# Kernel optimization log

Measured on AMD Instinct MI355X. Metric: run time of the kernel, lower is better.

The kernel has to match this reference:

```python
import jax, jax.numpy as jnp
import numpy as np

H, HKV, D, T, S, HID, I = 16, 8, 128, 2048, 4096, 2048, 8192
EPS = 1e-6
SCALE = 1.0 / (D ** 0.5)
NREP = H // HKV


def _rope_tables():
    inv_freq = 1.0 / (10000.0 ** (np.arange(0, D, 2, dtype=np.float32) / D))
    pos = np.arange(T, dtype=np.float32)
    freqs = np.outer(pos, inv_freq)            # (T, D/2)
    emb = np.concatenate([freqs, freqs], -1)   # (T, D)
    return jnp.asarray(np.cos(emb))[None], jnp.asarray(np.sin(emb))[None]


def setup_inputs() -> dict:
    key = jax.random.key(0)
    ks = jax.random.split(key, 8)
    w = 0.02
    cos, sin = _rope_tables()
    # causal mask over the full cache: query i may attend key j iff j <= i (current_pos=0)
    i = jnp.arange(T)[:, None]
    j = jnp.arange(S)[None, :]
    causal_mask = jnp.where(j <= i, 0.0, -1e9).astype(jnp.float32)[None, None]
    return {
        "hidden_conv": jax.random.normal(ks[0], (1, HID, 1, T), jnp.float32),
        "cos": cos, "sin": sin,
        "causal_mask": causal_mask,
        "kv_cache": jnp.zeros((2, HKV, S, D), jnp.float32),
        "wq": jax.random.normal(ks[1], (H * D, HID), jnp.float32) * w,
        "wk": jax.random.normal(ks[2], (HKV * D, HID), jnp.float32) * w,
        "wv": jax.random.normal(ks[3], (HKV * D, HID), jnp.float32) * w,
        "wo": jax.random.normal(ks[4], (H * D, HID), jnp.float32).T * w,  # (HID, H*D) stored as (out,in)
        "w_gate_up": jax.random.normal(ks[5], (2 * I, HID), jnp.float32) * w,
        "w_down": jax.random.normal(ks[6], (HID, I), jnp.float32) * w,
        "input_ln_w": jnp.ones((HID,), jnp.float32),
        "post_ln_w": jnp.ones((HID,), jnp.float32),
        "q_norm_w": jnp.ones((D,), jnp.float32),
        "k_norm_w": jnp.ones((D,), jnp.float32),
        "current_pos": 0,
    }


def _rms(x, w):
    return x * jax.lax.rsqrt(jnp.mean(x * x, axis=-1, keepdims=True) + EPS) * w


def _rot_half(x):
    x1, x2 = jnp.split(x, 2, axis=-1)
    return jnp.concatenate([-x2, x1], axis=-1)


def _layer(hidden_conv, cos, sin, causal_mask, kv_cache, wq, wk, wv, wo,
           w_gate_up, w_down, input_ln_w, post_ln_w, q_norm_w, k_norm_w, current_pos):
    x = hidden_conv[0, :, 0, :].T                       # (T, HID)
    h = _rms(x, input_ln_w)
    q = (h @ wq.T).reshape(T, H, D).transpose(1, 0, 2)   # (H, T, D)
    k = (h @ wk.T).reshape(T, HKV, D).transpose(1, 0, 2) # (HKV, T, D)
    v = (h @ wv.T).reshape(T, HKV, D).transpose(1, 0, 2)
    q = _rms(q, q_norm_w)
    k = _rms(k, k_norm_w)
    c, s = cos[0], sin[0]                                # (T, D)
    q = q * c + _rot_half(q) * s
    k = k * c + _rot_half(k) * s
    kv = kv_cache.at[0, :, current_pos:current_pos + T, :].set(k)
    kv = kv.at[1, :, current_pos:current_pos + T, :].set(v)
    k_rep = jnp.repeat(kv[0], NREP, axis=0)              # (H, S, D)
    v_rep = jnp.repeat(kv[1], NREP, axis=0)
    scores = jnp.einsum('htd,hsd->hts', q, k_rep) * SCALE + causal_mask[0, 0]
    attn = jax.nn.softmax(scores, axis=-1)
    out = jnp.einsum('hts,hsd->htd', attn, v_rep)        # (H, T, D)
    out = out.transpose(1, 0, 2).reshape(T, H * D)
    hidden = x + out @ wo.T
    h2 = _rms(hidden, post_ln_w)
    gu = h2 @ w_gate_up.T                                # (T, 2I)
    gate, up = gu[:, :I], gu[:, I:]
    hidden = hidden + (jax.nn.silu(gate) * up) @ w_down.T
    return hidden.T[None, :, None, :]                    # (1, HID, 1, T)


def reference(hidden_conv, cos, sin, causal_mask, kv_cache, wq, wk, wv, wo,
              w_gate_up, w_down, input_ln_w, post_ln_w, q_norm_w, k_norm_w, current_pos):
    return _layer(hidden_conv, cos, sin, causal_mask, kv_cache, wq, wk, wv, wo,
                  w_gate_up, w_down, input_ln_w, post_ln_w, q_norm_w, k_norm_w, current_pos)
```

## Files before the change

kernel.cpp:

```cpp
#include <hip/hip_runtime.h>
#include <hip/hip_bf16.h>
#include <stdint.h>

#define NHQ   16
#define NHKV  8
#define DH    128
#define TSEQ  2048
#define HIDN  2048
#define IMID  8192
#define EPS   1e-6f
#define SCL   0.08838834764831845f

typedef __attribute__((ext_vector_type(8))) short short8;
typedef __attribute__((ext_vector_type(4))) short short4v;
typedef __attribute__((ext_vector_type(4))) float f32x4;
typedef unsigned int u32;
typedef unsigned short u16;

__device__ __forceinline__ float b2f(short s) {
  union { u32 u; float f; } cv; cv.u = ((u32)(u16)s) << 16; return cv.f;
}
__device__ __forceinline__ short f2b(float f) {
  union { float f; u32 u; } cv; cv.f = f;
  u32 u = cv.u;
  u32 r = u + 0x7FFFu + ((u >> 16) & 1u);
  return (short)(r >> 16);
}

__device__ __forceinline__ void gll16(const void* g, void* l) {
  __builtin_amdgcn_global_load_lds(
      (const __attribute__((address_space(1))) u32*)g,
      (__attribute__((address_space(3))) u32*)l, 16, 0, 0);
}

__global__ __launch_bounds__(256)
void cvt_f2b(const float* __restrict__ in, short* __restrict__ out)
{
  const size_t i = ((size_t)blockIdx.x*256 + threadIdx.x)*8;
  f32x4 a0 = *(const f32x4*)(in + i);
  f32x4 a1 = *(const f32x4*)(in + i + 4);
  short8 y;
  #pragma unroll
  for (int j = 0; j < 4; ++j) { y[j] = f2b(a0[j]); y[j+4] = f2b(a1[j]); }
  *(short8*)(out + i) = y;
}

template<int EPI, bool BF32>
__global__ __launch_bounds__(256)
void gemm_bt(const short* __restrict__ A, int lda,
             const void* __restrict__ Bp,
             const void* __restrict__ RES,
             void* __restrict__ C, int N, int K)
{
  __shared__ __attribute__((aligned(16))) short As[128*64];
  __shared__ __attribute__((aligned(16))) short Bs[128*64];

  const int tid = threadIdx.x;
  const int wv = tid >> 6, ln = tid & 63;
  const int wm = wv >> 1, wn = wv & 1;
  const int l15 = ln & 15, quad = ln >> 4;
  const int bm0 = blockIdx.x * 128, bn0 = blockIdx.y * 128;

  f32x4 acc[4][4];
  #pragma unroll
  for (int i = 0; i < 4; ++i)
    #pragma unroll
    for (int j = 0; j < 4; ++j) acc[i][j] = (f32x4){0.f,0.f,0.f,0.f};

  const int srow = wv*32 + (ln >> 3);
  const int schk = ln & 7;
  const int brow = tid >> 4;
  const int bgrp = tid & 15;

  for (int kt = 0; kt < K; kt += 64) {
    #pragma unroll
    for (int i = 0; i < 4; ++i) {
      const int r = srow + i*8;
      const int g = schk ^ (r & 7);
      gll16(A + (size_t)(bm0 + r)*lda + kt + g*8,
            (char*)As + (wv*32 + i*8)*128);
      if (!BF32)
        gll16((const short*)Bp + (size_t)(bn0 + r)*K + kt + g*8,
              (char*)Bs + (wv*32 + i*8)*128);
    }
    if (BF32) {
      #pragma unroll
      for (int p = 0; p < 8; ++p) {
        const int r = p*16 + brow;
        f32x4 w4 = *(const f32x4*)((const float*)Bp + (size_t)(bn0 + r)*K + kt + bgrp*4);
        short4v s4;
        #pragma unroll
        for (int j = 0; j < 4; ++j) s4[j] = f2b(w4[j]);
        *(short4v*)(Bs + r*64 + (((bgrp >> 1) ^ (r & 7))*8) + (bgrp & 1)*4) = s4;
      }
    }
    __syncthreads();

    #pragma unroll
    for (int ks = 0; ks < 2; ++ks) {
      short8 af[4], bfr[4];
      #pragma unroll
      for (int mi = 0; mi < 4; ++mi) {
        const int r = wm*64 + mi*16 + l15;
        const int p = (quad + ks*4) ^ (r & 7);
        af[mi] = *(const short8*)(As + r*64 + p*8);
      }
      #pragma unroll
      for (int ni = 0; ni < 4; ++ni) {
        const int r = wn*64 + ni*16 + l15;
        const int p = (quad + ks*4) ^ (r & 7);
        bfr[ni] = *(const short8*)(Bs + r*64 + p*8);
      }
      #pragma unroll
      for (int mi = 0; mi < 4; ++mi)
        #pragma unroll
        for (int ni = 0; ni < 4; ++ni)
          acc[mi][ni] = __builtin_amdgcn_mfma_f32_16x16x32_bf16(
              af[mi], bfr[ni], acc[mi][ni], 0, 0, 0);
    }
    __syncthreads();
  }

  #pragma unroll
  for (int mi = 0; mi < 4; ++mi) {
    #pragma unroll
    for (int reg = 0; reg < 4; ++reg) {
      const int row = bm0 + wm*64 + mi*16 + quad*4 + reg;
      #pragma unroll
      for (int ni = 0; ni < 4; ++ni) {
        const int col = bn0 + wn*64 + ni*16 + l15;
        const size_t off = (size_t)row*N + col;
        const float v = acc[mi][ni][reg];
        if (EPI == 0)      ((short*)C)[off] = f2b(v);
        else if (EPI == 1) ((float*)C)[off] = b2f(((const short*)RES)[off]) + v;
        else               ((float*)C)[off] = ((const float*)RES)[off] + v;
      }
    }
  }
}

#define BAR256()   do { __builtin_amdgcn_s_barrier();                      \
                        __builtin_amdgcn_sched_barrier(0); } while (0)
#define LGKM0()    do { asm volatile("s_waitcnt lgkmcnt(0)" ::: "memory"); \
                        __builtin_amdgcn_sched_barrier(0); } while (0)
#define VMC4()     do { asm volatile("s_waitcnt vmcnt(4)" ::: "memory");   \
                        __builtin_amdgcn_sched_barrier(0); } while (0)

template<int EPI>
__global__ __launch_bounds__(512, 2)
void gemm256(const short* __restrict__ A, int lda,
             const short* __restrict__ B, int ldb,
             void* __restrict__ C, int N, int Ko)
{
  __shared__ __attribute__((aligned(16))) char L[131072];

  const int tid = threadIdx.x;
  const int wv = tid >> 6, ln = tid & 63;
  const int wm = wv >> 2, wn = wv & 3;
  const int l15 = ln & 15, quad = ln >> 4;

  int bx, by;
  {
    const int nwg  = gridDim.x * gridDim.y;
    const int orig = blockIdx.y * gridDim.x + blockIdx.x;
    const int wg   = (orig & 7) * (nwg >> 3) + (orig >> 3);
    bx = wg % gridDim.x;
    by = wg / gridDim.x;
  }
  const int bm0 = bx * 256, bn0 = by * 256;
  const int k0  = blockIdx.z * Ko;

  const int srow = wv*8 + (ln >> 3);
  const int g8   = ((ln & 7) ^ ((ln >> 3) & 7)) * 8;
  const short* Ab = A + (size_t)bm0 * lda + k0 + g8;
  const short* Bb = B + (size_t)bn0 * ldb + k0 + g8;

  const int aro = l15 * 128;
  const int p0  = ((quad    ) ^ (l15 & 7)) * 16;
  const int p1  = ((quad + 4) ^ (l15 & 7)) * 16;

  f32x4 acc[8][4];
  #pragma unroll
  for (int i = 0; i < 8; ++i)
    #pragma unroll
    for (int j = 0; j < 4; ++j) acc[i][j] = (f32x4){0.f,0.f,0.f,0.f};

  short8 af[4][2], bf0[2][2], bf1[2][2];

  const int NT = Ko >> 6;
  const int NI = NT >> 1;

#define STG(base, ld, s, h, t, isB)                                          \
  { char* r_ = L + (isB)*65536 + ((s)*2 + (h))*16384 + wv*1024;              \
    _Pragma("unroll")                                                        \
    for (int i_ = 0; i_ < 2; ++i_)                                           \
      gll16(base + (size_t)((h)*128 + i_*64 + srow)*(ld) + (size_t)(t)*64,   \
            r_ + i_*8192); }

#define LD_A(s, mh)                                                          \
  { const char* a_ = L + ((s)*2 + wm)*16384 + (mh)*8192 + aro;               \
    _Pragma("unroll")                                                        \
    for (int m_ = 0; m_ < 4; ++m_) {                                         \
      af[m_][0] = *(const short8*)(a_ + m_*2048 + p0);                       \
      af[m_][1] = *(const short8*)(a_ + m_*2048 + p1);                       \
    } }

#define LD_B(s, nh, bfv)                                                     \
  { const char* b_ = L + 65536 + ((s)*2 + (wn>>1))*16384 + (wn&1)*8192       \
                     + (nh)*4096 + aro;                                      \
    _Pragma("unroll")                                                        \
    for (int n_ = 0; n_ < 2; ++n_) {                                         \
      bfv[n_][0] = *(const short8*)(b_ + n_*2048 + p0);                      \
      bfv[n_][1] = *(const short8*)(b_ + n_*2048 + p1);                      \
    } }

#define MM_Q(mh, nh, bfv)                                                    \
  { __builtin_amdgcn_s_setprio(1);                                           \
    _Pragma("unroll")                                                        \
    for (int m_ = 0; m_ < 4; ++m_)                                           \
      _Pragma("unroll")                                                      \
      for (int n_ = 0; n_ < 2; ++n_) {                                       \
        acc[(mh)*4+m_][(nh)*2+n_] = __builtin_amdgcn_mfma_f32_16x16x32_bf16( \
            af[m_][0], bfv[n_][0], acc[(mh)*4+m_][(nh)*2+n_], 0, 0, 0);      \
        acc[(mh)*4+m_][(nh)*2+n_] = __builtin_amdgcn_mfma_f32_16x16x32_bf16( \
            af[m_][1], bfv[n_][1], acc[(mh)*4+m_][(nh)*2+n_], 0, 0, 0);      \
      }                                                                      \
    __builtin_amdgcn_s_setprio(0); }

  STG(Ab, lda, 0,0, 0, 0); STG(Ab, lda, 0,1, 0, 0);
  STG(Bb, ldb, 0,0, 0, 1); STG(Bb, ldb, 0,1, 0, 1);
  STG(Bb, ldb, 1,0, 1, 1); STG(Bb, ldb, 1,1, 1, 1);
  VMC4();
  BAR256();

  for (int it = 0; it < NI; ++it) {
    const int u   = it*2;
    const int tA1 = u + 1;
    const int t2  = (u+2 < NT) ? u+2 : NT-1;
    const int t3  = (u+3 < NT) ? u+3 : NT-1;

    LD_A(0,0); LD_B(0,0,bf0);
    STG(Ab, lda, 1,0, tA1, 0);
    BAR256(); LGKM0();
    MM_Q(0,0,bf0);
    BAR256();
    LD_B(0,1,bf1);
    STG(Ab, lda, 1,1, tA1, 0);
    BAR256(); LGKM0();
    MM_Q(0,1,bf1);
    BAR256();
    LD_A(0,1);
    STG(Bb, ldb, 0,0, t2, 1);
    BAR256(); LGKM0();
    MM_Q(1,0,bf0);
    BAR256();
    STG(Bb, ldb, 0,1, t2, 1);
    BAR256(); LGKM0();
    MM_Q(1,1,bf1);
    VMC4();
    BAR256();
    LD_A(1,0); LD_B(1,0,bf0);
    STG(Ab, lda, 0,0, t2, 0);
    BAR256(); LGKM0();
    MM_Q(0,0,bf0);
    BAR256();
    LD_B(1,1,bf1);
    STG(Ab, lda, 0,1, t2, 0);
    BAR256(); LGKM0();
    MM_Q(0,1,bf1);
    BAR256();
    LD_A(1,1);
    STG(Bb, ldb, 1,0, t3, 1);
    BAR256(); LGKM0();
    MM_Q(1,0,bf0);
    BAR256();
    STG(Bb, ldb, 1,1, t3, 1);
    BAR256(); LGKM0();
    MM_Q(1,1,bf1);
    VMC4();
    BAR256();
  }

  #pragma unroll
  for (int mi = 0; mi < 8; ++mi) {
    #pragma unroll
    for (int reg = 0; reg < 4; ++reg) {
      const int row = bm0 + wm*128 + mi*16 + quad*4 + reg;
      #pragma unroll
      for (int ni = 0; ni < 4; ++ni) {
        const int col = bn0 + wn*64 + ni*16 + l15;
        const size_t off = (size_t)row*N + col;
        const float v = acc[mi][ni][reg];
        if (EPI == 0) ((short*)C)[off] = f2b(v);
        else          atomicAdd((float*)C + off, v);
      }
    }
  }
#undef STG
#undef LD_A
#undef LD_B
#undef MM_Q
}

__global__ __launch_bounds__(256)
void transpose_f2b(const float* __restrict__ in, short* __restrict__ out,
                   int rows_in, int cols_in)
{
  __shared__ float tile[64][65];
  const int c0 = blockIdx.x*64, r0 = blockIdx.y*64;
  const int tx = threadIdx.x & 63, ty = threadIdx.x >> 6;
  #pragma unroll
  for (int i = 0; i < 16; ++i) {
    const int r = ty + i*4;
    tile[r][tx] = in[(size_t)(r0+r)*cols_in + c0 + tx];
  }
  __syncthreads();
  #pragma unroll
  for (int i = 0; i < 16; ++i) {
    const int r = ty + i*4;
    out[(size_t)(c0+r)*rows_in + r0 + tx] = f2b(tile[tx][r]);
  }
}

__global__ __launch_bounds__(256)
void transpose_f2f(const float* __restrict__ in, float* __restrict__ out,
                   int rows_in, int cols_in)
{
  __shared__ float tile[64][65];
  const int c0 = blockIdx.x*64, r0 = blockIdx.y*64;
  const int tx = threadIdx.x & 63, ty = threadIdx.x >> 6;
  #pragma unroll
  for (int i = 0; i < 16; ++i) {
    const int r = ty + i*4;
    tile[r][tx] = in[(size_t)(r0+r)*cols_in + c0 + tx];
  }
  __syncthreads();
  #pragma unroll
  for (int i = 0; i < 16; ++i) {
    const int r = ty + i*4;
    out[(size_t)(c0+r)*rows_in + r0 + tx] = tile[tx][r];
  }
}

__global__ __launch_bounds__(256)
void rmsnorm_b(const short* __restrict__ X, const float* __restrict__ W,
               short* __restrict__ Y)
{
  const int row = blockIdx.x, tid = threadIdx.x;
  const int wv = tid >> 6, ln = tid & 63;
  const size_t base = (size_t)row*HIDN + tid*8;
  short8 xv = *(const short8*)(X + base);
  float x[8];
  #pragma unroll
  for (int j = 0; j < 8; ++j) x[j] = b2f(xv[j]);
  float s = 0.f;
  #pragma unroll
  for (int j = 0; j < 8; ++j) s += x[j]*x[j];
  #pragma unroll
  for (int off = 32; off; off >>= 1) s += __shfl_xor(s, off, 64);
  __shared__ float red[4];
  if (ln == 0) red[wv] = s;
  __syncthreads();
  const float tot = red[0]+red[1]+red[2]+red[3];
  const float r = rsqrtf(tot*(1.0f/HIDN) + EPS);
  f32x4 w0 = *(const f32x4*)(W + tid*8);
  f32x4 w1 = *(const f32x4*)(W + tid*8 + 4);
  short8 y;
  #pragma unroll
  for (int j = 0; j < 4; ++j) y[j]   = f2b(x[j]*r*w0[j]);
  #pragma unroll
  for (int j = 0; j < 4; ++j) y[j+4] = f2b(x[j+4]*r*w1[j]);
  *(short8*)(Y + base) = y;
}

__global__ __launch_bounds__(256)
void rmsnorm_f(const float* __restrict__ X, const float* __restrict__ W,
               short* __restrict__ Y)
{
  const int row = blockIdx.x, tid = threadIdx.x;
  const int wv = tid >> 6, ln = tid & 63;
  const size_t base = (size_t)row*HIDN + tid*8;
  f32x4 a0 = *(const f32x4*)(X + base);
  f32x4 a1 = *(const f32x4*)(X + base + 4);
  float x[8] = {a0[0],a0[1],a0[2],a0[3],a1[0],a1[1],a1[2],a1[3]};
  float s = 0.f;
  #pragma unroll
  for (int j = 0; j < 8; ++j) s += x[j]*x[j];
  #pragma unroll
  for (int off = 32; off; off >>= 1) s += __shfl_xor(s, off, 64);
  __shared__ float red[4];
  if (ln == 0) red[wv] = s;
  __syncthreads();
  const float tot = red[0]+red[1]+red[2]+red[3];
  const float r = rsqrtf(tot*(1.0f/HIDN) + EPS);
  f32x4 w0 = *(const f32x4*)(W + tid*8);
  f32x4 w1 = *(const f32x4*)(W + tid*8 + 4);
  short8 y;
  #pragma unroll
  for (int j = 0; j < 4; ++j) y[j]   = f2b(x[j]*r*w0[j]);
  #pragma unroll
  for (int j = 0; j < 4; ++j) y[j+4] = f2b(x[j+4]*r*w1[j]);
  *(short8*)(Y + base) = y;
}

__global__ __launch_bounds__(64)
void qk_rms_rope(short* __restrict__ Qb, short* __restrict__ Kb,
                 const float* __restrict__ cosb, const float* __restrict__ sinb,
                 const float* __restrict__ qw, const float* __restrict__ kw)
{
  const int b = blockIdx.x;
  const int hi = b % (NHQ + NHKV);
  const int t  = b / (NHQ + NHKV);
  const int ln = threadIdx.x;
  short* row; const float* w;
  if (hi < NHQ) { row = Qb + (size_t)t*(NHQ*DH) + hi*DH; w = qw; }
  else          { row = Kb + (size_t)t*(NHKV*DH) + (hi-NHQ)*DH; w = kw; }
  float x0 = b2f(row[ln]), x1 = b2f(row[ln+64]);
  float s = x0*x0 + x1*x1;
  #pragma unroll
  for (int off = 32; off; off >>= 1) s += __shfl_xor(s, off, 64);
  const float r = rsqrtf(s*(1.0f/DH) + EPS);
  const float n0 = x0*r*w[ln];
  const float n1 = x1*r*w[ln+64];
  const float* cr = cosb + (size_t)t*DH;
  const float* sr = sinb + (size_t)t*DH;
  const float c0 = cr[ln], c1 = cr[ln+64];
  const float s0 = sr[ln], s1 = sr[ln+64];
  row[ln]    = f2b(n0*c0 - n1*s0);
  row[ln+64] = f2b(n1*c1 + n0*s1);
}

__global__ __launch_bounds__(256)
void flash_attn(const short* __restrict__ Q, const short* __restrict__ Kb,
                const short* __restrict__ Vb, short* __restrict__ O)
{
  __shared__ __attribute__((aligned(16))) short Ks[64*128];
  __shared__ __attribute__((aligned(16))) short Vt[128*64];
  __shared__ __attribute__((aligned(16))) short Ps[4*16*64];

  const int tid = threadIdx.x, wv = tid >> 6, ln = tid & 63;
  const int l15 = ln & 15, quad = ln >> 4;
  const int hh = blockIdx.y, kvh = hh >> 1;
  const int nbx = gridDim.x;
  const int bxr = blockIdx.x;
  const int bx  = (bxr & 1) ? (nbx - 1 - (bxr >> 1)) : (bxr >> 1);
  const int m0 = bx * 64;
  const int qm0 = m0 + wv*16;

  short8 qf[4];
  {
    const short* qb = Q + (size_t)(qm0 + l15)*(NHQ*DH) + hh*DH + quad*8;
    #pragma unroll
    for (int ks = 0; ks < 4; ++ks) qf[ks] = *(const short8*)(qb + ks*32);
  }

  f32x4 oa[8];
  #pragma unroll
  for (int i = 0; i < 8; ++i) oa[i] = (f32x4){0.f,0.f,0.f,0.f};
  float m_r[4] = {-1e30f,-1e30f,-1e30f,-1e30f};
  float l_r[4] = {0.f,0.f,0.f,0.f};

  const int l7 = l15 & 7;

  const int ntile = bx + 1;
  for (int st = 0; st < ntile; ++st) {
    const int s0 = st*64;
    __syncthreads();

    #pragma unroll
    for (int it = 0; it < 4; ++it) {
      const int r = (wv*4 + it)*4 + quad;
      const int g = l15 ^ (4*(it & 1) + quad);
      gll16(Kb + (size_t)(s0 + r)*(NHKV*DH) + kvh*DH + g*8,
            (char*)Ks + (wv*4 + it)*1024);
    }
    {
      const int d = tid & 127, sh = tid >> 7;
      #pragma unroll
      for (int cb = 0; cb < 4; ++cb) {
        short8 t8;
        #pragma unroll
        for (int j = 0; j < 8; ++j)
          t8[j] = Vb[(size_t)(s0 + sh*32 + cb*8 + j)*(NHKV*DH) + kvh*DH + d];
        *(short8*)(Vt + d*64 + (((sh*4 + cb) ^ (d & 7))*8)) = t8;
      }
    }
    __syncthreads();

    f32x4 sc[4];
    #pragma unroll
    for (int ci = 0; ci < 4; ++ci) {
      f32x4 a = (f32x4){0.f,0.f,0.f,0.f};
      #pragma unroll
      for (int ks = 0; ks < 4; ++ks) {
        const int r = ci*16 + l15;
        const int p = (quad + ks*4) ^ l7;
        short8 kf = *(const short8*)(Ks + r*128 + p*8);
        a = __builtin_amdgcn_mfma_f32_16x16x32_bf16(qf[ks], kf, a, 0, 0, 0);
      }
      sc[ci] = a;
    }

    float alpha[4];
    #pragma unroll
    for (int reg = 0; reg < 4; ++reg) {
      const int grow = qm0 + quad*4 + reg;
      float rmax = -1e30f;
      #pragma unroll
      for (int ci = 0; ci < 4; ++ci) {
        float v = sc[ci][reg]*SCL;
        const int gs = s0 + ci*16 + l15;
        v = (gs <= grow) ? v : -1e30f;
        sc[ci][reg] = v;
        rmax = fmaxf(rmax, v);
      }
      #pragma unroll
      for (int off = 1; off < 16; off <<= 1)
        rmax = fmaxf(rmax, __shfl_xor(rmax, off, 64));
      const float mn = fmaxf(m_r[reg], rmax);
      alpha[reg] = __expf(m_r[reg] - mn);
      m_r[reg] = mn;
      float rsum = 0.f;
      #pragma unroll
      for (int ci = 0; ci < 4; ++ci) {
        const float p = __expf(sc[ci][reg] - mn);
        sc[ci][reg] = p;
        rsum += p;
      }
      #pragma unroll
      for (int off = 1; off < 16; off <<= 1)
        rsum += __shfl_xor(rsum, off, 64);
      l_r[reg] = l_r[reg]*alpha[reg] + rsum;
    }
    #pragma unroll
    for (int ni = 0; ni < 8; ++ni)
      #pragma unroll
      for (int reg = 0; reg < 4; ++reg) oa[ni][reg] *= alpha[reg];

    #pragma unroll
    for (int ci = 0; ci < 4; ++ci)
      #pragma unroll
      for (int reg = 0; reg < 4; ++reg) {
        const int row = quad*4 + reg;
        const int pc  = (ci*2 + (l15 >> 3)) ^ (row & 7);
        Ps[wv*1024 + row*64 + pc*8 + l7] = f2b(sc[ci][reg]);
      }

    __syncthreads();

    #pragma unroll
    for (int ks = 0; ks < 2; ++ks) {
      const int gp = quad + ks*4;
      const int pp = gp ^ l7;
      short8 pf = *(const short8*)(Ps + wv*1024 + l15*64 + pp*8);
      #pragma unroll
      for (int ni = 0; ni < 8; ++ni) {
        const int d = ni*16 + l15;
        short8 vf = *(const short8*)(Vt + d*64 + ((gp ^ l7)*8));
        oa[ni] = __builtin_amdgcn_mfma_f32_16x16x32_bf16(pf, vf, oa[ni], 0, 0, 0);
      }
    }
  }

  #pragma unroll
  for (int reg = 0; reg < 4; ++reg) {
    const float inv = 1.0f / l_r[reg];
    const int row = qm0 + quad*4 + reg;
    #pragma unroll
    for (int ni = 0; ni < 8; ++ni)
      O[(size_t)row*(NHQ*DH) + hh*DH + ni*16 + l15] = f2b(oa[ni][reg]*inv);
  }
}

__global__ __launch_bounds__(256)
void silu_mul(short* __restrict__ gu)
{
  const size_t idx = ((size_t)blockIdx.x*256 + threadIdx.x)*8;
  const size_t t = idx / IMID;
  const size_t i = idx % IMID;
  short* gp = gu + t*(2*IMID) + i;
  short8 g8 = *(const short8*)gp;
  short8 u8 = *(const short8*)(gp + IMID);
  short8 o;
  #pragma unroll
  for (int j = 0; j < 8; ++j) {
    const float g = b2f(g8[j]);
    const float u = b2f(u8[j]);
    const float sl = g / (1.f + __expf(-g));
    o[j] = f2b(sl*u);
  }
  *(short8*)gp = o;
}

extern "C" void kernel_launch(void* const* d_in, const int* in_sizes, int n_in,
                              void* d_out, int out_size, void* d_ws, size_t ws_size,
                              hipStream_t stream)
{
  const float* hc   = (const float*)d_in[0];
  const float* cosb = (const float*)d_in[1];
  const float* sinb = (const float*)d_in[2];
  const float* wq   = (const float*)d_in[5];
  const float* wk   = (const float*)d_in[6];
  const float* wvp  = (const float*)d_in[7];
  const float* wo   = (const float*)d_in[8];
  const float* wgu  = (const float*)d_in[9];
  const float* wdn  = (const float*)d_in[10];
  const float* iln  = (const float*)d_in[11];
  const float* pln  = (const float*)d_in[12];
  const float* qnw  = (const float*)d_in[13];
  const float* knw  = (const float*)d_in[14];

  char* ws = (char*)d_ws;
  short* wgu_b = (short*)(ws);
  short* wq_b  = (short*)(ws + ((size_t)64 << 20));
  short* wk_b  = (short*)(ws + ((size_t)72 << 20));
  short* wv_b  = (short*)(ws + ((size_t)76 << 20));
  short* wo_b  = (short*)(ws + ((size_t)80 << 20));
  short* xT    = (short*)(ws + ((size_t)88 << 20));
  short* h     = (short*)(ws + ((size_t)96 << 20));
  short* q     = (short*)(ws + ((size_t)104 << 20));
  short* k     = (short*)(ws + ((size_t)112 << 20));
  short* v     = (short*)(ws + ((size_t)116 << 20));
  short* ao    = (short*)(ws + ((size_t)120 << 20));
  float* hid   = (float*)(ws + ((size_t)104 << 20));
  short* h2    = (short*)(ws + ((size_t)120 << 20));
  short* gu    = (short*)(ws + ((size_t)128 << 20));
  short* wdn_b = (short*)(ws + ((size_t)64 << 20));

  const dim3 b256(256);
  const dim3 b512(512);

  cvt_f2b<<<dim3(16384), b256, 0, stream>>>(wgu, wgu_b);
  cvt_f2b<<<dim3(2048),  b256, 0, stream>>>(wq,  wq_b);
  cvt_f2b<<<dim3(1024),  b256, 0, stream>>>(wk,  wk_b);
  cvt_f2b<<<dim3(1024),  b256, 0, stream>>>(wvp, wv_b);
  cvt_f2b<<<dim3(2048),  b256, 0, stream>>>(wo,  wo_b);

  transpose_f2b<<<dim3(32,32), b256, 0, stream>>>(hc, xT, HIDN, TSEQ);
  rmsnorm_b<<<dim3(TSEQ), b256, 0, stream>>>(xT, iln, h);

  gemm_bt<0,false><<<dim3(16,16), b256, 0, stream>>>(h, HIDN, wq_b, nullptr, q, 2048, 2048);
  gemm_bt<0,false><<<dim3(16,8),  b256, 0, stream>>>(h, HIDN, wk_b, nullptr, k, 1024, 2048);
  gemm_bt<0,false><<<dim3(16,8),  b256, 0, stream>>>(h, HIDN, wv_b, nullptr, v, 1024, 2048);

  qk_rms_rope<<<dim3(TSEQ*(NHQ+NHKV)), dim3(64), 0, stream>>>(q, k, cosb, sinb, qnw, knw);

  flash_attn<<<dim3(TSEQ/64, NHQ), b256, 0, stream>>>(q, k, v, ao);

  gemm_bt<1,false><<<dim3(16,16), b256, 0, stream>>>(ao, 2048, wo_b, xT, hid, 2048, 2048);

  cvt_f2b<<<dim3(8192), b256, 0, stream>>>(wdn, wdn_b);

  rmsnorm_f<<<dim3(TSEQ), b256, 0, stream>>>(hid, pln, h2);

  gemm256<0><<<dim3(8,64), b512, 0, stream>>>(h2, HIDN, wgu_b, HIDN, gu, 16384, 2048);
  silu_mul<<<dim3((TSEQ*IMID/8)/256), b256, 0, stream>>>(gu);
  gemm256<3><<<dim3(8,8,4), b512, 0, stream>>>(gu, 2*IMID, wdn_b, IMID, hid, 2048, 2048);

  transpose_f2f<<<dim3(32,32), b256, 0, stream>>>(hid, (float*)d_out, TSEQ, HIDN);
}
```

Before: 879.1 us.

## Fuse QKV GEMMs, double-buffer flash attention, replace split-K atomics with partial reduce

Merges the three Q/K/V projection GEMMs into one launch that routes each column tile to its output. Flash attention now double-buffers the K and V shared-memory tiles and prefetches the next tile while computing the current one. It also drops one barrier per iteration. The split-K down projection writes plain partial sums to a workspace instead of using float atomics, and a fused reduce-transpose kernel adds the residual and the four partials. The partial buffer reuses workspace at offset 0, where the bf16 gate/up weights live, and this is only safe because that GEMM has already finished.

```diff
diff --git a/kernel.cpp b/kernel.cpp
--- a/kernel.cpp
+++ b/kernel.cpp
@@ -134,6 +134,86 @@
         if (EPI == 0)      ((short*)C)[off] = f2b(v);
         else if (EPI == 1) ((float*)C)[off] = b2f(((const short*)RES)[off]) + v;
         else               ((float*)C)[off] = ((const float*)RES)[off] + v;
+      }
+    }
+  }
+}
+
+__global__ __launch_bounds__(256)
+void gemm_qkv(const short* __restrict__ A,
+              const short* __restrict__ Bq, const short* __restrict__ Bk,
+              const short* __restrict__ Bv,
+              short* __restrict__ q, short* __restrict__ k, short* __restrict__ v)
+{
+  __shared__ __attribute__((aligned(16))) short As[128*64];
+  __shared__ __attribute__((aligned(16))) short Bs[128*64];
+
+  const int tid = threadIdx.x;
+  const int wv = tid >> 6, ln = tid & 63;
+  const int wm = wv >> 1, wn = wv & 1;
+  const int l15 = ln & 15, quad = ln >> 4;
+  const int bm0 = blockIdx.x * 128, bn0 = blockIdx.y * 128;
+
+  const short* Bp; short* C; int ldc, cb0;
+  if (bn0 < 2048)      { Bp = Bq + (size_t)bn0*HIDN;        C = q; ldc = 2048; cb0 = bn0; }
+  else if (bn0 < 3072) { Bp = Bk + (size_t)(bn0-2048)*HIDN; C = k; ldc = 1024; cb0 = bn0-2048; }
+  else                 { Bp = Bv + (size_t)(bn0-3072)*HIDN; C = v; ldc = 1024; cb0 = bn0-3072; }
+
+  f32x4 acc[4][4];
+  #pragma unroll
+  for (int i = 0; i < 4; ++i)
+    #pragma unroll
+    for (int j = 0; j < 4; ++j) acc[i][j] = (f32x4){0.f,0.f,0.f,0.f};
+
+  const int srow = wv*32 + (ln >> 3);
+  const int schk = ln & 7;
+
+  for (int kt = 0; kt < HIDN; kt += 64) {
+    #pragma unroll
+    for (int i = 0; i < 4; ++i) {
+      const int r = srow + i*8;
+      const int g = schk ^ (r & 7);
+      gll16(A + (size_t)(bm0 + r)*HIDN + kt + g*8,
+            (char*)As + (wv*32 + i*8)*128);
+      gll16(Bp + (size_t)r*HIDN + kt + g*8,
+            (char*)Bs + (wv*32 + i*8)*128);
+    }
+    __syncthreads();
+
+    #pragma unroll
+    for (int ks = 0; ks < 2; ++ks) {
+      short8 af[4], bfr[4];
+      #pragma unroll
+      for (int mi = 0; mi < 4; ++mi) {
+        const int r = wm*64 + mi*16 + l15;
+        const int p = (quad + ks*4) ^ (r & 7);
+        af[mi] = *(const short8*)(As + r*64 + p*8);
+      }
+      #pragma unroll
+      for (int ni = 0; ni < 4; ++ni) {
+        const int r = wn*64 + ni*16 + l15;
+        const int p = (quad + ks*4) ^ (r & 7);
+        bfr[ni] = *(const short8*)(Bs + r*64 + p*8);
+      }
+      #pragma unroll
+      for (int mi = 0; mi < 4; ++mi)
+        #pragma unroll
+        for (int ni = 0; ni < 4; ++ni)
+          acc[mi][ni] = __builtin_amdgcn_mfma_f32_16x16x32_bf16(
+              af[mi], bfr[ni], acc[mi][ni], 0, 0, 0);
+    }
+    __syncthreads();
+  }
+
+  #pragma unroll
+  for (int mi = 0; mi < 4; ++mi) {
+    #pragma unroll
+    for (int reg = 0; reg < 4; ++reg) {
+      const int row = bm0 + wm*64 + mi*16 + quad*4 + reg;
+      #pragma unroll
+      for (int ni = 0; ni < 4; ++ni) {
+        const int col = cb0 + wn*64 + ni*16 + l15;
+        C[(size_t)row*ldc + col] = f2b(acc[mi][ni][reg]);
       }
     }
   }
@@ -244,36 +324,43 @@
     BAR256(); LGKM0();
     MM_Q(0,0,bf0);
     BAR256();
+
     LD_B(0,1,bf1);
     STG(Ab, lda, 1,1, tA1, 0);
     BAR256(); LGKM0();
     MM_Q(0,1,bf1);
     BAR256();
+
     LD_A(0,1);
     STG(Bb, ldb, 0,0, t2, 1);
     BAR256(); LGKM0();
     MM_Q(1,0,bf0);
     BAR256();
+
     STG(Bb, ldb, 0,1, t2, 1);
     BAR256(); LGKM0();
     MM_Q(1,1,bf1);
     VMC4();
     BAR256();
+
     LD_A(1,0); LD_B(1,0,bf0);
     STG(Ab, lda, 0,0, t2, 0);
     BAR256(); LGKM0();
     MM_Q(0,0,bf0);
     BAR256();
+
     LD_B(1,1,bf1);
     STG(Ab, lda, 0,1, t2, 0);
     BAR256(); LGKM0();
     MM_Q(0,1,bf1);
     BAR256();
+
     LD_A(1,1);
     STG(Bb, ldb, 1,0, t3, 1);
     BAR256(); LGKM0();
     MM_Q(1,0,bf0);
     BAR256();
+
     STG(Bb, ldb, 1,1, t3, 1);
     BAR256(); LGKM0();
     MM_Q(1,1,bf1);
@@ -292,7 +379,7 @@
         const size_t off = (size_t)row*N + col;
         const float v = acc[mi][ni][reg];
         if (EPI == 0) ((short*)C)[off] = f2b(v);
-        else          atomicAdd((float*)C + off, v);
+        else          ((float*)C)[(size_t)blockIdx.z*(2048u*2048u) + off] = v;
       }
     }
   }
@@ -323,8 +410,8 @@
 }
 
 __global__ __launch_bounds__(256)
-void transpose_f2f(const float* __restrict__ in, float* __restrict__ out,
-                   int rows_in, int cols_in)
+void reduce_transpose(const float* __restrict__ hid, const float* __restrict__ part,
+                      float* __restrict__ out)
 {
   __shared__ float tile[64][65];
   const int c0 = blockIdx.x*64, r0 = blockIdx.y*64;
@@ -332,13 +419,15 @@
   #pragma unroll
   for (int i = 0; i < 16; ++i) {
     const int r = ty + i*4;
-    tile[r][tx] = in[(size_t)(r0+r)*cols_in + c0 + tx];
+    const size_t off = (size_t)(r0+r)*HIDN + c0 + tx;
+    tile[r][tx] = hid[off] + part[off] + part[off + 4194304u]
+                + part[off + 2u*4194304u] + part[off + 3u*4194304u];
   }
   __syncthreads();
   #pragma unroll
   for (int i = 0; i < 16; ++i) {
     const int r = ty + i*4;
-    out[(size_t)(c0+r)*rows_in + r0 + tx] = tile[tx][r];
+    out[(size_t)(c0+r)*TSEQ + r0 + tx] = tile[tx][r];
   }
 }
 
@@ -434,12 +523,13 @@
 void flash_attn(const short* __restrict__ Q, const short* __restrict__ Kb,
                 const short* __restrict__ Vb, short* __restrict__ O)
 {
-  __shared__ __attribute__((aligned(16))) short Ks[64*128];
-  __shared__ __attribute__((aligned(16))) short Vt[128*64];
+  __shared__ __attribute__((aligned(16))) short Ks[2][64*128];
+  __shared__ __attribute__((aligned(16))) short Vt[2][128*64];
   __shared__ __attribute__((aligned(16))) short Ps[4*16*64];
 
   const int tid = threadIdx.x, wv = tid >> 6, ln = tid & 63;
   const int l15 = ln & 15, quad = ln >> 4;
+  const int l7 = l15 & 7;
   const int hh = blockIdx.y, kvh = hh >> 1;
   const int nbx = gridDim.x;
   const int bxr = blockIdx.x;
@@ -460,32 +550,49 @@
   float m_r[4] = {-1e30f,-1e30f,-1e30f,-1e30f};
   float l_r[4] = {0.f,0.f,0.f,0.f};
 
-  const int l7 = l15 & 7;
-
-  const int ntile = bx + 1;
-  for (int st = 0; st < ntile; ++st) {
-    const int s0 = st*64;
-    __syncthreads();
-
+  const int vd = tid & 127, vsh = tid >> 7;
+  short8 vreg[4];
+
+  {
+    #pragma unroll
+    for (int cb = 0; cb < 4; ++cb)
+      #pragma unroll
+      for (int j = 0; j < 8; ++j)
+        vreg[cb][j] = Vb[(size_t)(vsh*32 + cb*8 + j)*(NHKV*DH) + kvh*DH + vd];
     #pragma unroll
     for (int it = 0; it < 4; ++it) {
       const int r = (wv*4 + it)*4 + quad;
       const int g = l15 ^ (4*(it & 1) + quad);
-      gll16(Kb + (size_t)(s0 + r)*(NHKV*DH) + kvh*DH + g*8,
-            (char*)Ks + (wv*4 + it)*1024);
-    }
-    {
-      const int d = tid & 127, sh = tid >> 7;
-      #pragma unroll
-      for (int cb = 0; cb < 4; ++cb) {
-        short8 t8;
+      gll16(Kb + (size_t)r*(NHKV*DH) + kvh*DH + g*8,
+            (char*)Ks[0] + (wv*4 + it)*1024);
+    }
+    #pragma unroll
+    for (int cb = 0; cb < 4; ++cb)
+      *(short8*)(Vt[0] + vd*64 + (((vsh*4 + cb) ^ (vd & 7))*8)) = vreg[cb];
+    __syncthreads();
+  }
+
+  const int ntile = bx + 1;
+  for (int t = 0; t < ntile; ++t) {
+    const int cur = t & 1, nxt = cur ^ 1;
+    const int s0 = t*64;
+    const bool pf = (t + 1 < ntile);
+
+    if (pf) {
+      const int s1 = s0 + 64;
+      #pragma unroll
+      for (int cb = 0; cb < 4; ++cb)
         #pragma unroll
         for (int j = 0; j < 8; ++j)
-          t8[j] = Vb[(size_t)(s0 + sh*32 + cb*8 + j)*(NHKV*DH) + kvh*DH + d];
-        *(short8*)(Vt + d*64 + (((sh*4 + cb) ^ (d & 7))*8)) = t8;
-      }
-    }
-    __syncthreads();
+          vreg[cb][j] = Vb[(size_t)(s1 + vsh*32 + cb*8 + j)*(NHKV*DH) + kvh*DH + vd];
+      #pragma unroll
+      for (int it = 0; it < 4; ++it) {
+        const int r = (wv*4 + it)*4 + quad;
+        const int g = l15 ^ (4*(it & 1) + quad);
+        gll16(Kb + (size_t)(s1 + r)*(NHKV*DH) + kvh*DH + g*8,
+              (char*)Ks[nxt] + (wv*4 + it)*1024);
+      }
+    }
 
     f32x4 sc[4];
     #pragma unroll
@@ -495,7 +602,7 @@
       for (int ks = 0; ks < 4; ++ks) {
         const int r = ci*16 + l15;
         const int p = (quad + ks*4) ^ l7;
-        short8 kf = *(const short8*)(Ks + r*128 + p*8);
+        short8 kf = *(const short8*)(Ks[cur] + r*128 + p*8);
         a = __builtin_amdgcn_mfma_f32_16x16x32_bf16(qf[ks], kf, a, 0, 0, 0);
       }
       sc[ci] = a;
@@ -508,11 +615,11 @@
       float rmax = -1e30f;
       #pragma unroll
       for (int ci = 0; ci < 4; ++ci) {
-        float v = sc[ci][reg]*SCL;
+        float vvv = sc[ci][reg]*SCL;
         const int gs = s0 + ci*16 + l15;
-        v = (gs <= grow) ? v : -1e30f;
-        sc[ci][reg] = v;
-        rmax = fmaxf(rmax, v);
+        vvv = (gs <= grow) ? vvv : -1e30f;
+        sc[ci][reg] = vvv;
+        rmax = fmaxf(rmax, vvv);
       }
       #pragma unroll
       for (int off = 1; off < 16; off <<= 1)
@@ -546,20 +653,25 @@
         Ps[wv*1024 + row*64 + pc*8 + l7] = f2b(sc[ci][reg]);
       }
 
-    __syncthreads();
-
     #pragma unroll
     for (int ks = 0; ks < 2; ++ks) {
       const int gp = quad + ks*4;
       const int pp = gp ^ l7;
-      short8 pf = *(const short8*)(Ps + wv*1024 + l15*64 + pp*8);
+      short8 pf8 = *(const short8*)(Ps + wv*1024 + l15*64 + pp*8);
       #pragma unroll
       for (int ni = 0; ni < 8; ++ni) {
         const int d = ni*16 + l15;
-        short8 vf = *(const short8*)(Vt + d*64 + ((gp ^ l7)*8));
-        oa[ni] = __builtin_amdgcn_mfma_f32_16x16x32_bf16(pf, vf, oa[ni], 0, 0, 0);
-      }
-    }
+        short8 vf = *(const short8*)(Vt[cur] + d*64 + ((gp ^ l7)*8));
+        oa[ni] = __builtin_amdgcn_mfma_f32_16x16x32_bf16(pf8, vf, oa[ni], 0, 0, 0);
+      }
+    }
+
+    if (pf) {
+      #pragma unroll
+      for (int cb = 0; cb < 4; ++cb)
+        *(short8*)(Vt[nxt] + vd*64 + (((vsh*4 + cb) ^ (vd & 7))*8)) = vreg[cb];
+    }
+    __syncthreads();
   }
 
   #pragma unroll
@@ -626,6 +738,7 @@
   short* h2    = (short*)(ws + ((size_t)120 << 20));
   short* gu    = (short*)(ws + ((size_t)128 << 20));
   short* wdn_b = (short*)(ws + ((size_t)64 << 20));
+  float* part  = (float*)(ws);
 
   const dim3 b256(256);
   const dim3 b512(512);
@@ -639,9 +752,7 @@
   transpose_f2b<<<dim3(32,32), b256, 0, stream>>>(hc, xT, HIDN, TSEQ);
   rmsnorm_b<<<dim3(TSEQ), b256, 0, stream>>>(xT, iln, h);
 
-  gemm_bt<0,false><<<dim3(16,16), b256, 0, stream>>>(h, HIDN, wq_b, nullptr, q, 2048, 2048);
-  gemm_bt<0,false><<<dim3(16,8),  b256, 0, stream>>>(h, HIDN, wk_b, nullptr, k, 1024, 2048);
-  gemm_bt<0,false><<<dim3(16,8),  b256, 0, stream>>>(h, HIDN, wv_b, nullptr, v, 1024, 2048);
+  gemm_qkv<<<dim3(16,32), b256, 0, stream>>>(h, wq_b, wk_b, wv_b, q, k, v);
 
   qk_rms_rope<<<dim3(TSEQ*(NHQ+NHKV)), dim3(64), 0, stream>>>(q, k, cosb, sinb, qnw, knw);
 
@@ -655,7 +766,7 @@
 
   gemm256<0><<<dim3(8,64), b512, 0, stream>>>(h2, HIDN, wgu_b, HIDN, gu, 16384, 2048);
   silu_mul<<<dim3((TSEQ*IMID/8)/256), b256, 0, stream>>>(gu);
-  gemm256<3><<<dim3(8,8,4), b512, 0, stream>>>(gu, 2*IMID, wdn_b, IMID, hid, 2048, 2048);
-
-  transpose_f2f<<<dim3(32,32), b256, 0, stream>>>(hid, (float*)d_out, TSEQ, HIDN);
-}
+  gemm256<4><<<dim3(8,8,4), b512, 0, stream>>>(gu, 2*IMID, wdn_b, IMID, part, 2048, 2048);
+
+  reduce_transpose<<<dim3(32,32), b256, 0, stream>>>(hid, part, (float*)d_out);
+}
```

Result: faster. 753.3 us (-14.3%).
